# Kernel tuning notes

Hardware: AMD Instinct MI355X
Metric: run time of the kernel (lower is better)

## Reference

```python
import jax, jax.numpy as jnp
import numpy as np

N = 20000
H = 256
W = 256
CHUNK = 500  # N must be divisible by CHUNK
CHOL_BOUND = np.array([0.5, 0.0, 0.5], dtype=np.float32)


def setup_inputs() -> dict:
    key = jax.random.key(0)
    k1, k2, k3 = jax.random.split(key, 3)
    return {
        "_xyz": jax.random.normal(k1, (N, 2), dtype=jnp.float32),
        "_cholesky": jax.random.uniform(k2, (N, 3), dtype=jnp.float32),
        "_features_dc": jax.random.uniform(k3, (N, 3), dtype=jnp.float32),
        "rgb_W": jnp.ones((N, 1), dtype=jnp.float32),
    }


def _render(_xyz, _cholesky, _features_dc, rgb_W):
    # --- project_gaussians_2d ---
    xy = jnp.tanh(_xyz)                                  # [N,2] in (-1,1)
    chol = _cholesky + jnp.asarray(CHOL_BOUND)           # [N,3] (l1,l2,l3)
    l1, l2, l3 = chol[:, 0], chol[:, 1], chol[:, 2]
    # Sigma = L L^T,  L = [[l1,0],[l2,l3]]
    s11 = l1 * l1
    s12 = l1 * l2
    s22 = l2 * l2 + l3 * l3
    det = s11 * s22 - s12 * s12
    conic_a = s22 / det
    conic_b = -s12 / det
    conic_c = s11 / det
    # pixel-space centers
    cx = 0.5 * W * (xy[:, 0] + 1.0) - 0.5                # [N]
    cy = 0.5 * H * (xy[:, 1] + 1.0) - 0.5                # [N]
    feats = _features_dc * rgb_W                         # [N,3]; opacity = 1

    px = jnp.arange(W, dtype=jnp.float32)                # [W]
    py = jnp.arange(H, dtype=jnp.float32)                # [H]

    n_chunks = N // CHUNK
    params = (
        cx.reshape(n_chunks, CHUNK),
        cy.reshape(n_chunks, CHUNK),
        conic_a.reshape(n_chunks, CHUNK),
        conic_b.reshape(n_chunks, CHUNK),
        conic_c.reshape(n_chunks, CHUNK),
        feats.reshape(n_chunks, CHUNK, 3),
    )

    def body(img, p):
        ccx, ccy, ca, cb, cc, cf = p
        dx = px[None, :] - ccx[:, None]                  # [C,W]
        dy = py[None, :] - ccy[:, None]                  # [C,H]
        # sigma = 0.5*(a*dx^2 + c*dy^2) + b*dx*dy  -> [C,H,W]
        sigma = (0.5 * (ca[:, None] * dx * dx))[:, None, :] \
              + (0.5 * (cc[:, None] * dy * dy))[:, :, None] \
              + (cb[:, None] * dy)[:, :, None] * dx[:, None, :]
        w = jnp.exp(-jnp.maximum(sigma, 0.0))            # [C,H,W]
        img = img + jnp.einsum("chw,cf->hwf", w, cf)
        return img, None

    img0 = jnp.zeros((H, W, 3), dtype=jnp.float32)
    img, _ = jax.lax.scan(body, img0, params)
    out = jnp.clip(img, 0.0, 1.0)                        # [H,W,3]
    return out.reshape(1, H, W, 3).transpose(0, 3, 1, 2)  # [1,3,H,W]


def reference(_xyz, _cholesky, _features_dc, rgb_W):
    return _render(_xyz, _cholesky, _features_dc, rgb_W)
```

## Files before the change

kernel.cpp:

```cpp
#include <hip/hip_runtime.h>


#define N_G   20000
#define IMG_H 256
#define IMG_W 256
#define TILE  16
#define TILES_X (IMG_W / TILE)
#define TILES_Y (IMG_H / TILE)
#define CUT_T 18.0f

__global__ __launch_bounds__(256) void gs_preprocess(
    const float* __restrict__ xyz,
    const float* __restrict__ chol,
    const float* __restrict__ fdc,
    const float* __restrict__ rgbw,
    float4* __restrict__ bbox,
    float4* __restrict__ p0,
    float4* __restrict__ p1)
{
    int gi = blockIdx.x * 256 + threadIdx.x;
    if (gi >= N_G) return;
    float l1 = chol[3 * gi + 0] + 0.5f;
    float l2 = chol[3 * gi + 1];
    float l3 = chol[3 * gi + 2] + 0.5f;
    float s11 = l1 * l1;
    float s12 = l1 * l2;
    float s22 = l2 * l2 + l3 * l3;
    float det = s11 * s22 - s12 * s12;
    float inv = 1.0f / det;
    float ca = s22 * inv;
    float cb = -s12 * inv;
    float cc = s11 * inv;
    float cx = 0.5f * (float)IMG_W * (tanhf(xyz[2 * gi + 0]) + 1.0f) - 0.5f;
    float cy = 0.5f * (float)IMG_H * (tanhf(xyz[2 * gi + 1]) + 1.0f) - 0.5f;
    float rx = sqrtf(2.0f * CUT_T * s11);
    float ry = sqrtf(2.0f * CUT_T * s22);
    float wgt = rgbw[gi];
    bbox[gi] = make_float4(cx - rx, cx + rx, cy - ry, cy + ry);
    p0[gi] = make_float4(cx, cy, ca, cb);
    p1[gi] = make_float4(cc, fdc[3 * gi + 0] * wgt, fdc[3 * gi + 1] * wgt,
                         fdc[3 * gi + 2] * wgt);
}

__global__ __launch_bounds__(256) void gs_tiles(
    const float4* __restrict__ bbox,
    const float4* __restrict__ p0,
    const float4* __restrict__ p1,
    float* __restrict__ partial,
    int g_per_slice)
{
    __shared__ float4 sh0[256];
    __shared__ float4 sh1[256];
    __shared__ int cnt;

    const int tid = threadIdx.x;
    const int tile = blockIdx.x;
    const int slice = blockIdx.y;
    const int tx0 = (tile % TILES_X) * TILE;
    const int ty0 = (tile / TILES_X) * TILE;
    const int px = tx0 + (tid & (TILE - 1));
    const int py = ty0 + (tid >> 4);
    const float pxf = (float)px;
    const float pyf = (float)py;
    const float txmin = (float)tx0, txmax = (float)(tx0 + TILE - 1);
    const float tymin = (float)ty0, tymax = (float)(ty0 + TILE - 1);

    const int g0 = slice * g_per_slice;
    const int g1 = min(N_G, g0 + g_per_slice);

    float ar = 0.0f, ag = 0.0f, ab = 0.0f;

    for (int base = g0; base < g1; base += 256) {
        __syncthreads();
        if (tid == 0) cnt = 0;
        __syncthreads();
        int gi = base + tid;
        if (gi < g1) {
            float4 bb = bbox[gi];
            if (bb.x <= txmax && bb.y >= txmin && bb.z <= tymax && bb.w >= tymin) {
                int slot = atomicAdd(&cnt, 1);
                sh0[slot] = p0[gi];
                sh1[slot] = p1[gi];
            }
        }
        __syncthreads();
        int m = cnt;
        for (int j = 0; j < m; ++j) {
            float4 q0 = sh0[j];
            float4 q1 = sh1[j];
            float dx = pxf - q0.x;
            float dy = pyf - q0.y;
            float sigma = 0.5f * (q0.z * dx * dx + q1.x * dy * dy) + q0.w * dx * dy;
            float w = __expf(-fmaxf(sigma, 0.0f));
            ar = fmaf(w, q1.y, ar);
            ag = fmaf(w, q1.z, ag);
            ab = fmaf(w, q1.w, ab);
        }
    }

    const size_t plane = (size_t)IMG_H * IMG_W;
    float* dst = partial + (size_t)slice * 3 * plane + (size_t)py * IMG_W + px;
    dst[0] = ar;
    dst[plane] = ag;
    dst[2 * plane] = ab;
}

__global__ __launch_bounds__(256) void gs_reduce(
    const float* __restrict__ partial, float* __restrict__ out, int slices)
{
    const int total = 3 * IMG_H * IMG_W;
    int i = blockIdx.x * 256 + threadIdx.x;
    if (i >= total) return;
    float s = 0.0f;
    for (int sl = 0; sl < slices; ++sl)
        s += partial[(size_t)sl * total + i];
    out[i] = fminf(fmaxf(s, 0.0f), 1.0f);
}

extern "C" void kernel_launch(void* const* d_in, const int* in_sizes, int n_in,
                              void* d_out, int out_size, void* d_ws, size_t ws_size,
                              hipStream_t stream) {
    const float* xyz  = (const float*)d_in[0];
    const float* chol = (const float*)d_in[1];
    const float* fdc  = (const float*)d_in[2];
    const float* rgbw = (const float*)d_in[3];
    float* out = (float*)d_out;

    char* ws = (char*)d_ws;
    float4* bbox = (float4*)(ws);
    float4* p0   = (float4*)(ws + (size_t)N_G * 16);
    float4* p1   = (float4*)(ws + (size_t)N_G * 32);
    float* partial = (float*)(ws + (size_t)N_G * 48);

    const size_t gbytes = (size_t)N_G * 48;
    const size_t per_slice = (size_t)3 * IMG_H * IMG_W * sizeof(float);
    int slices = 8;
    while (slices > 1 && gbytes + (size_t)slices * per_slice > ws_size)
        slices >>= 1;
    int gps = (N_G + slices - 1) / slices;

    gs_preprocess<<<(N_G + 255) / 256, 256, 0, stream>>>(
        xyz, chol, fdc, rgbw, bbox, p0, p1);
    gs_tiles<<<dim3(TILES_X * TILES_Y, slices), 256, 0, stream>>>(
        bbox, p0, p1, partial, gps);
    gs_reduce<<<(3 * IMG_H * IMG_W + 255) / 256, 256, 0, stream>>>(
        partial, out, slices);
}
```

Before: 85.55 us.

## Assign one wavefront per tile with readlane broadcast and 4 pixels per lane

Restructures the tile kernel so each 64-lane wavefront handles a whole 16x16 tile, with each lane computing four pixels. Gaussians are culled with a ballot and broadcast through readlane instead of LDS compaction with atomics and block barriers. The next batch is prefetched into registers while the current one is processed. Constants are prescaled by log2(e) so the kernel can use exp2, the slice count rises to 16, and the reduce kernel is vectorised with float4. This gives more work per lane and removes shared-memory synchronisation, at the cost of higher register pressure and a serial per-wavefront loop over visible Gaussians.

```diff
diff --git a/kernel.cpp b/kernel.cpp
--- a/kernel.cpp
+++ b/kernel.cpp
@@ -5,18 +5,23 @@
 #define IMG_H 256
 #define IMG_W 256
 #define TILE  16
-#define TILES_X (IMG_W / TILE)
-#define TILES_Y (IMG_H / TILE)
+#define NTILES 256
+#define MAX_SLICES 16
 #define CUT_T 18.0f
+#define LOG2E 1.4426950408889634f
+
+__device__ __forceinline__ float rl(float v, int j) {
+    return __int_as_float(__builtin_amdgcn_readlane(__float_as_int(v), j));
+}
 
 __global__ __launch_bounds__(256) void gs_preprocess(
     const float* __restrict__ xyz,
     const float* __restrict__ chol,
     const float* __restrict__ fdc,
     const float* __restrict__ rgbw,
-    float4* __restrict__ bbox,
-    float4* __restrict__ p0,
-    float4* __restrict__ p1)
+    float4* __restrict__ a0,
+    float4* __restrict__ a1,
+    float4* __restrict__ a2)
 {
     int gi = blockIdx.x * 256 + threadIdx.x;
     if (gi >= N_G) return;
@@ -36,85 +41,107 @@
     float rx = sqrtf(2.0f * CUT_T * s11);
     float ry = sqrtf(2.0f * CUT_T * s22);
     float wgt = rgbw[gi];
-    bbox[gi] = make_float4(cx - rx, cx + rx, cy - ry, cy + ry);
-    p0[gi] = make_float4(cx, cy, ca, cb);
-    p1[gi] = make_float4(cc, fdc[3 * gi + 0] * wgt, fdc[3 * gi + 1] * wgt,
-                         fdc[3 * gi + 2] * wgt);
+    a0[gi] = make_float4(cx - rx, cx + rx, cy - ry, cy + ry);
+    a1[gi] = make_float4(cx, cy, 0.5f * ca * LOG2E, cb * LOG2E);
+    a2[gi] = make_float4(0.5f * cc * LOG2E, fdc[3 * gi + 0] * wgt,
+                         fdc[3 * gi + 1] * wgt, fdc[3 * gi + 2] * wgt);
 }
 
 __global__ __launch_bounds__(256) void gs_tiles(
-    const float4* __restrict__ bbox,
-    const float4* __restrict__ p0,
-    const float4* __restrict__ p1,
+    const float4* __restrict__ a0,
+    const float4* __restrict__ a1,
+    const float4* __restrict__ a2,
     float* __restrict__ partial,
     int g_per_slice)
 {
-    __shared__ float4 sh0[256];
-    __shared__ float4 sh1[256];
-    __shared__ int cnt;
-
-    const int tid = threadIdx.x;
-    const int tile = blockIdx.x;
-    const int slice = blockIdx.y;
-    const int tx0 = (tile % TILES_X) * TILE;
-    const int ty0 = (tile / TILES_X) * TILE;
-    const int px = tx0 + (tid & (TILE - 1));
-    const int py = ty0 + (tid >> 4);
-    const float pxf = (float)px;
-    const float pyf = (float)py;
+    const int tid  = threadIdx.x;
+    const int lane = tid & 63;
+    const int task = blockIdx.x * 4 + (tid >> 6);
+    const int tile = task & (NTILES - 1);
+    const int slice = task >> 8;
+    const int tx0 = (tile & 15) * TILE;
+    const int ty0 = (tile >> 4) * TILE;
+    const float pxf = (float)(tx0 + (lane & 15));
+    const float py0 = (float)(ty0 + ((lane >> 4) << 2));
     const float txmin = (float)tx0, txmax = (float)(tx0 + TILE - 1);
     const float tymin = (float)ty0, tymax = (float)(ty0 + TILE - 1);
 
     const int g0 = slice * g_per_slice;
     const int g1 = min(N_G, g0 + g_per_slice);
 
-    float ar = 0.0f, ag = 0.0f, ab = 0.0f;
+    float acc[12];
+    #pragma unroll
+    for (int i = 0; i < 12; ++i) acc[i] = 0.0f;
 
-    for (int base = g0; base < g1; base += 256) {
-        __syncthreads();
-        if (tid == 0) cnt = 0;
-        __syncthreads();
-        int gi = base + tid;
-        if (gi < g1) {
-            float4 bb = bbox[gi];
-            if (bb.x <= txmax && bb.y >= txmin && bb.z <= tymax && bb.w >= tymin) {
-                int slot = atomicAdd(&cnt, 1);
-                sh0[slot] = p0[gi];
-                sh1[slot] = p1[gi];
+    int gi = g0 + lane;
+    float4 bb = make_float4(1.e30f, -1.e30f, 1.e30f, -1.e30f);
+    float4 v1 = make_float4(0, 0, 0, 0), v2 = make_float4(0, 0, 0, 0);
+    if (gi < g1) { bb = a0[gi]; v1 = a1[gi]; v2 = a2[gi]; }
+
+    for (int base = g0; base < g1; base += 64) {
+        bool ok = (base + lane < g1) &&
+                  bb.x <= txmax && bb.y >= txmin && bb.z <= tymax && bb.w >= tymin;
+        unsigned long long mask = __ballot(ok);
+
+        float4 nbb = bb, nv1 = v1, nv2 = v2;
+        int ngi = base + 64 + lane;
+        if (base + 64 < g1) {
+            if (ngi < g1) { nbb = a0[ngi]; nv1 = a1[ngi]; nv2 = a2[ngi]; }
+            else nbb = make_float4(1.e30f, -1.e30f, 1.e30f, -1.e30f);
+        }
+
+        while (mask) {
+            int j = __ffsll((unsigned long long)mask) - 1;
+            mask &= mask - 1;
+            float cx  = rl(v1.x, j), cy  = rl(v1.y, j);
+            float cah = rl(v1.z, j), cbs = rl(v1.w, j);
+            float cch = rl(v2.x, j);
+            float fr  = rl(v2.y, j), fg = rl(v2.z, j), fb = rl(v2.w, j);
+            float dx  = pxf - cx;
+            float t0  = cah * dx * dx;
+            float bdx = cbs * dx;
+            #pragma unroll
+            for (int k = 0; k < 4; ++k) {
+                float dy = (py0 + (float)k) - cy;
+                float s  = fmaf(cch * dy, dy, fmaf(bdx, dy, t0));
+                float w  = exp2f(-fmaxf(s, 0.0f));
+                acc[3 * k + 0] = fmaf(w, fr, acc[3 * k + 0]);
+                acc[3 * k + 1] = fmaf(w, fg, acc[3 * k + 1]);
+                acc[3 * k + 2] = fmaf(w, fb, acc[3 * k + 2]);
             }
         }
-        __syncthreads();
-        int m = cnt;
-        for (int j = 0; j < m; ++j) {
-            float4 q0 = sh0[j];
-            float4 q1 = sh1[j];
-            float dx = pxf - q0.x;
-            float dy = pyf - q0.y;
-            float sigma = 0.5f * (q0.z * dx * dx + q1.x * dy * dy) + q0.w * dx * dy;
-            float w = __expf(-fmaxf(sigma, 0.0f));
-            ar = fmaf(w, q1.y, ar);
-            ag = fmaf(w, q1.z, ag);
-            ab = fmaf(w, q1.w, ab);
-        }
+        bb = nbb; v1 = nv1; v2 = nv2;
     }
 
-    const size_t plane = (size_t)IMG_H * IMG_W;
-    float* dst = partial + (size_t)slice * 3 * plane + (size_t)py * IMG_W + px;
-    dst[0] = ar;
-    dst[plane] = ag;
-    dst[2 * plane] = ab;
+    const int plane = IMG_H * IMG_W;
+    float* dst = partial + (size_t)slice * 3 * plane;
+    const int x = tx0 + (lane & 15);
+    const int y0i = ty0 + ((lane >> 4) << 2);
+    #pragma unroll
+    for (int k = 0; k < 4; ++k) {
+        int pix = (y0i + k) * IMG_W + x;
+        dst[pix] = acc[3 * k + 0];
+        dst[plane + pix] = acc[3 * k + 1];
+        dst[2 * plane + pix] = acc[3 * k + 2];
+    }
 }
 
 __global__ __launch_bounds__(256) void gs_reduce(
-    const float* __restrict__ partial, float* __restrict__ out, int slices)
+    const float4* __restrict__ partial, float4* __restrict__ out, int slices)
 {
-    const int total = 3 * IMG_H * IMG_W;
+    const int total4 = 3 * IMG_H * IMG_W / 4;
     int i = blockIdx.x * 256 + threadIdx.x;
-    if (i >= total) return;
-    float s = 0.0f;
-    for (int sl = 0; sl < slices; ++sl)
-        s += partial[(size_t)sl * total + i];
-    out[i] = fminf(fmaxf(s, 0.0f), 1.0f);
+    if (i >= total4) return;
+    float4 s = make_float4(0, 0, 0, 0);
+    for (int sl = 0; sl < slices; ++sl) {
+        float4 p = partial[(size_t)sl * total4 + i];
+        s.x += p.x; s.y += p.y; s.z += p.z; s.w += p.w;
+    }
+    s.x = fminf(fmaxf(s.x, 0.0f), 1.0f);
+    s.y = fminf(fmaxf(s.y, 0.0f), 1.0f);
+    s.z = fminf(fmaxf(s.z, 0.0f), 1.0f);
+    s.w = fminf(fmaxf(s.w, 0.0f), 1.0f);
+    out[i] = s;
 }
 
 extern "C" void kernel_launch(void* const* d_in, const int* in_sizes, int n_in,
@@ -124,25 +151,24 @@
     const float* chol = (const float*)d_in[1];
     const float* fdc  = (const float*)d_in[2];
     const float* rgbw = (const float*)d_in[3];
-    float* out = (float*)d_out;
 
     char* ws = (char*)d_ws;
-    float4* bbox = (float4*)(ws);
-    float4* p0   = (float4*)(ws + (size_t)N_G * 16);
-    float4* p1   = (float4*)(ws + (size_t)N_G * 32);
-    float* partial = (float*)(ws + (size_t)N_G * 48);
+    float4* a0 = (float4*)(ws);
+    float4* a1 = (float4*)(ws + (size_t)N_G * 16);
+    float4* a2 = (float4*)(ws + (size_t)N_G * 32);
+    float*  partial = (float*)(ws + (size_t)N_G * 48);
 
     const size_t gbytes = (size_t)N_G * 48;
     const size_t per_slice = (size_t)3 * IMG_H * IMG_W * sizeof(float);
-    int slices = 8;
+    int slices = MAX_SLICES;
     while (slices > 1 && gbytes + (size_t)slices * per_slice > ws_size)
         slices >>= 1;
     int gps = (N_G + slices - 1) / slices;
 
     gs_preprocess<<<(N_G + 255) / 256, 256, 0, stream>>>(
-        xyz, chol, fdc, rgbw, bbox, p0, p1);
-    gs_tiles<<<dim3(TILES_X * TILES_Y, slices), 256, 0, stream>>>(
-        bbox, p0, p1, partial, gps);
-    gs_reduce<<<(3 * IMG_H * IMG_W + 255) / 256, 256, 0, stream>>>(
-        partial, out, slices);
+        xyz, chol, fdc, rgbw, a0, a1, a2);
+    gs_tiles<<<(NTILES * slices) / 4, 256, 0, stream>>>(
+        a0, a1, a2, partial, gps);
+    gs_reduce<<<(3 * IMG_H * IMG_W / 4 + 255) / 256, 256, 0, stream>>>(
+        (const float4*)partial, (float4*)d_out, slices);
 }
```

Result: slower. 91.81 us (+7.3%).
